# Performance work log

Hardware: AMD Instinct MI355X
Metric: run time of the kernel (lower is better)

Reference implementation:

```python
import jax, jax.numpy as jnp
import numpy as np

SIZE = 5
N_RADIAL = 4
EPS = 1e-5
PAD = [(3, 3)] * 3
# (scalar_in, scalar_out, vector) per Block, from features=[1,8,16,16,16,10]
DIMS = [(1, 8, 4), (8, 16, 12), (16, 16, 16), (16, 16, 16), (16, 10, 13)]


def _basis():
    # 5^3 grid of offsets, radial hat basis and angular (Cartesian) basis tensors
    o = jnp.arange(SIZE, dtype=jnp.float32) - (SIZE - 1) / 2.0
    X, Y, Z = jnp.meshgrid(o, o, o, indexing='ij')
    r = jnp.sqrt(X ** 2 + Y ** 2 + Z ** 2)
    hats = jnp.stack([jnp.clip(1.0 - jnp.abs(r - k), 0.0, None) for k in range(N_RADIAL)])  # [K,5,5,5]
    inv = jnp.where(r > 0, 1.0 / jnp.where(r > 0, r, 1.0), 0.0)
    xhat = jnp.stack([X * inv, Y * inv, Z * inv])  # [3,5,5,5], zero at origin
    mask = (r > 0).astype(jnp.float32)
    eye = jnp.eye(3, dtype=jnp.float32)
    e = np.zeros((3, 3, 3), np.float32)
    e[0, 1, 2] = e[1, 2, 0] = e[2, 0, 1] = 1.0
    e[0, 2, 1] = e[2, 1, 0] = e[1, 0, 2] = -1.0
    eps3 = jnp.asarray(e)
    a0 = eye[:, :, None, None, None] * jnp.ones_like(r)                      # J=0: delta_ij
    a1 = jnp.einsum('ijl,lxyz->ijxyz', eps3, xhat)                           # J=1: eps_ijl xhat_l
    a2 = xhat[:, None] * xhat[None, :] - eye[:, :, None, None, None] / 3.0 * mask  # J=2 traceless sym
    ang = jnp.stack([a0, a1, a2])  # [3,3,3,5,5,5]
    return hats, xhat, ang


def _conv(x, K, stride):
    return jax.lax.conv_general_dilated(x, K, (stride,) * 3, PAD,
                                        dimension_numbers=('NCDHW', 'OIDHW', 'NCDHW'))


def _bn3d(x, gamma, beta):
    m = x.mean((0, 2, 3, 4), keepdims=True)
    v = x.var((0, 2, 3, 4), keepdims=True)
    xn = (x - m) * jax.lax.rsqrt(v + EPS)
    return xn * gamma[None, :, None, None, None] + beta[None, :, None, None, None]


def _block(s, w1, wA, wB, bias, gamma, beta, relu, hats, xhat, ang):
    vec, s_in = w1.shape[0], w1.shape[1]
    s_out = wA.shape[0]
    # conv1: scalar -> vector, equivariant kernel K1[o*3+j, i] = xhat_j * sum_k w1[o,i,k] hat_k(r)
    R1 = jnp.einsum('oik,kxyz->oixyz', w1, hats)
    K1 = (xhat[None, :, None] * R1[:, None]).reshape(vec * 3, s_in, SIZE, SIZE, SIZE)
    v = _conv(s, K1, 2)  # [B, vec*3, D,H,W]
    B = v.shape[0]
    sp = v.shape[2:]
    # TensorProduct: per-channel outer product v_i v_j -> repr3x3 (9 comps)
    vr = v.reshape(B, vec, 3, *sp)
    t = (vr[:, :, :, None] * vr[:, :, None, :]).reshape(B, vec * 9, *sp)
    vt = jnp.concatenate([v, t], axis=1)
    # conv2: (repr3 ++ repr3x3) -> scalar
    RA = jnp.einsum('ovk,kxyz->ovxyz', wA, hats)
    KA = (RA[:, :, None] * xhat[None, None]).reshape(s_out, vec * 3, SIZE, SIZE, SIZE)
    RB = jnp.einsum('ovmk,kxyz->ovmxyz', wB, hats)
    KB = jnp.einsum('ovmxyz,mijxyz->ovijxyz', RB, ang).reshape(s_out, vec * 9, SIZE, SIZE, SIZE)
    K2 = jnp.concatenate([KA, KB], axis=1)
    out = _conv(vt, K2, 1)
    out = _bn3d(out, gamma, beta)  # scalar_batch_norm=True
    if relu:  # bias_relu flag
        out = jax.nn.relu(out + bias[None, :, None, None, None])
    return out


def _forward(x, params, gamma_out, beta_out):
    hats, xhat, ang = _basis()
    # bn_in, affine=False
    m = x.mean((0, 2, 3, 4), keepdims=True)
    v = x.var((0, 2, 3, 4), keepdims=True)
    s = (x - m) * jax.lax.rsqrt(v + EPS)
    n = len(params)
    for i, (w1, wA, wB, bias, gamma, beta) in enumerate(params):
        s = _block(s, w1, wA, wB, bias, gamma, beta, i < n - 1, hats, xhat, ang)
    pooled = s.mean((2, 3, 4))  # global average pool -> [B, classes]
    m = pooled.mean(0)
    v = pooled.var(0)
    return gamma_out * (pooled - m) * jax.lax.rsqrt(v + EPS) + beta_out


def setup_inputs() -> dict:
    key = jax.random.key(0)
    ks = iter(jax.random.split(key, 64))
    inp = {'x': jax.random.normal(next(ks), (32, 1, 64, 64, 64), dtype=jnp.float32)}
    for i, (si, so, ve) in enumerate(DIMS):
        inp[f'w1_{i}'] = jax.random.normal(next(ks), (ve, si, N_RADIAL), dtype=jnp.float32) * (si * 125) ** -0.5
        inp[f'wA_{i}'] = jax.random.normal(next(ks), (so, ve, N_RADIAL), dtype=jnp.float32) * (ve * 3 * 125) ** -0.5
        inp[f'wB_{i}'] = jax.random.normal(next(ks), (so, ve, 3, N_RADIAL), dtype=jnp.float32) * (ve * 9 * 125) ** -0.5
        inp[f'bias_{i}'] = jnp.zeros((so,), jnp.float32)
        inp[f'gamma_{i}'] = jnp.ones((so,), jnp.float32)
        inp[f'beta_{i}'] = jnp.zeros((so,), jnp.float32)
    inp['gamma_out'] = jnp.ones((10,), jnp.float32)
    inp['beta_out'] = jnp.zeros((10,), jnp.float32)
    return inp


def reference(x, w1_0, wA_0, wB_0, bias_0, gamma_0, beta_0,
              w1_1, wA_1, wB_1, bias_1, gamma_1, beta_1,
              w1_2, wA_2, wB_2, bias_2, gamma_2, beta_2,
              w1_3, wA_3, wB_3, bias_3, gamma_3, beta_3,
              w1_4, wA_4, wB_4, bias_4, gamma_4, beta_4,
              gamma_out, beta_out):
    params = [
        (w1_0, wA_0, wB_0, bias_0, gamma_0, beta_0),
        (w1_1, wA_1, wB_1, bias_1, gamma_1, beta_1),
        (w1_2, wA_2, wB_2, bias_2, gamma_2, beta_2),
        (w1_3, wA_3, wB_3, bias_3, gamma_3, beta_3),
        (w1_4, wA_4, wB_4, bias_4, gamma_4, beta_4),
    ]
    return _forward(x, params, gamma_out, beta_out)
```

## Files before the change

### kernel.cpp

```cpp
#include <hip/hip_runtime.h>
#include <math.h>

#define EPSF 1e-5f

typedef _Float16 f16;
typedef __attribute__((ext_vector_type(8))) _Float16 f16x8;
typedef __attribute__((ext_vector_type(4))) float f32x4;

__device__ __forceinline__ void tap_geom(int tap, float hats[4], float xh[3], float& mask) {
  int d = tap / 25, h = (tap / 5) % 5, w = tap % 5;
  float X = (float)(d - 2), Y = (float)(h - 2), Z = (float)(w - 2);
  float r = sqrtf(X * X + Y * Y + Z * Z);
#pragma unroll
  for (int k = 0; k < 4; ++k) hats[k] = fmaxf(1.0f - fabsf(r - (float)k), 0.0f);
  float inv = (r > 0.0f) ? (1.0f / r) : 0.0f;
  xh[0] = X * inv; xh[1] = Y * inv; xh[2] = Z * inv;
  mask = (r > 0.0f) ? 1.0f : 0.0f;
}

__global__ void build_k1(const float* __restrict__ w1, float* __restrict__ K1,
                         int VEC, int SIN) {
  int total = SIN * 125 * VEC;
  for (int idx = blockIdx.x * blockDim.x + threadIdx.x; idx < total;
       idx += gridDim.x * blockDim.x) {
    int cv = idx % VEC;
    int tap = (idx / VEC) % 125;
    int i = idx / (VEC * 125);
    float hats[4], xh[3], mask;
    tap_geom(tap, hats, xh, mask);
    float R = 0.f;
#pragma unroll
    for (int k = 0; k < 4; ++k) R += w1[(cv * SIN + i) * 4 + k] * hats[k];
    float* o = K1 + (long)idx * 4;
    o[0] = xh[0] * R; o[1] = xh[1] * R; o[2] = xh[2] * R; o[3] = 0.f;
  }
}

__global__ void build_k2c(const float* __restrict__ wA, const float* __restrict__ wB,
                          f16* __restrict__ K2, int VEC, int SOUT, int KS) {
  int total = 125 * KS * 64 * 8;
  for (int idx = blockIdx.x * blockDim.x + threadIdx.x; idx < total;
       idx += gridDim.x * blockDim.x) {
    int e = idx & 7;
    int lane = (idx >> 3) & 63;
    int ks = (idx >> 9) % KS;
    int tap = idx / (KS << 9);
    int n = lane & 15;
    int g = lane >> 4;
    int c = (ks * 4 + g) * 8 + e;
    float val = 0.f;
    if (n < SOUT && c < VEC * 12) {
      float hats[4], xh[3], mask;
      tap_geom(tap, hats, xh, mask);
      int cv = c / 12, comp = c % 12;
      if (comp < 3) {
        float RA = 0.f;
#pragma unroll
        for (int k = 0; k < 4; ++k) RA += wA[(n * VEC + cv) * 4 + k] * hats[k];
        val = RA * xh[comp];
      } else {
        int ij = comp - 3;
        int ii = ij / 3, jj = ij % 3;
        float RB[3];
#pragma unroll
        for (int m = 0; m < 3; ++m) {
          float r = 0.f;
#pragma unroll
          for (int k = 0; k < 4; ++k) r += wB[((n * VEC + cv) * 3 + m) * 4 + k] * hats[k];
          RB[m] = r;
        }
        float a0 = (ii == jj) ? 1.0f : 0.0f;
        float a1 = 0.0f;
        if (ii != jj) {
          int l = 3 - ii - jj;
          float sgn = (((jj - ii + 3) % 3) == 1) ? 1.0f : -1.0f;
          a1 = sgn * xh[l];
        }
        float a2 = xh[ii] * xh[jj] - ((ii == jj) ? (mask / 3.0f) : 0.0f);
        val = RB[0] * a0 + RB[1] * a1 + RB[2] * a2;
      }
    }
    K2[idx] = (f16)val;
  }
}

template <int SIN, int VEC, int CP8>
__global__ __launch_bounds__(256) void conv1_vt_x(const float* __restrict__ s,
                                                  const f32x4* __restrict__ K1,
                                                  f16* __restrict__ VT,
                                                  int Bc, int IS, int OS, int XG) {
  constexpr int NP = (VEC + 1) / 2;
  int iss = IS * IS * IS;
  long total = (long)Bc * OS * OS * XG * NP;
  for (long idx = blockIdx.x * (long)blockDim.x + threadIdx.x; idx < total;
       idx += gridDim.x * (long)blockDim.x) {
    int xg = (int)(idx % XG);
    int pp = (int)((idx / XG) % NP);
    int y  = (int)((idx / ((long)XG * NP)) % OS);
    int z  = (int)((idx / ((long)XG * NP * OS)) % OS);
    int b  = (int)(idx / ((long)XG * NP * OS * OS));
    int x0 = xg * 4;
    int cv0 = 2 * pp;
    int cv1 = (2 * pp + 1 < VEC) ? (2 * pp + 1) : (VEC - 1);

    float acc[2][3][4];
#pragma unroll
    for (int p = 0; p < 2; ++p)
#pragma unroll
      for (int c = 0; c < 3; ++c)
#pragma unroll
        for (int t = 0; t < 4; ++t) acc[p][c][t] = 0.f;

    const float* sb = s + (long)b * SIN * iss;
    const f32x4* kb = K1;
    for (int i = 0; i < SIN; ++i) {
      for (int d = 0; d < 5; ++d) {
        int iz = 2 * z - 3 + d;
        if ((unsigned)iz >= (unsigned)IS) continue;
        for (int h = 0; h < 5; ++h) {
          int iy = 2 * y - 3 + h;
          if ((unsigned)iy >= (unsigned)IS) continue;
          const float* srow = sb + (iz * IS + iy) * IS;
          float sv[11];
#pragma unroll
          for (int m = 0; m < 11; ++m) {
            int xi = 2 * x0 - 3 + m;
            bool ok = (unsigned)xi < (unsigned)IS;
            sv[m] = ok ? srow[ok ? xi : 0] : 0.f;
          }
          const f32x4* krow = kb + (d * 25 + h * 5) * VEC;
#pragma unroll
          for (int w = 0; w < 5; ++w) {
            f32x4 k0 = krow[w * VEC + cv0];
            f32x4 k1 = krow[w * VEC + cv1];
#pragma unroll
            for (int t = 0; t < 4; ++t) {
              float sx = sv[2 * t + w];
              acc[0][0][t] = fmaf(sx, k0[0], acc[0][0][t]);
              acc[0][1][t] = fmaf(sx, k0[1], acc[0][1][t]);
              acc[0][2][t] = fmaf(sx, k0[2], acc[0][2][t]);
              acc[1][0][t] = fmaf(sx, k1[0], acc[1][0][t]);
              acc[1][1][t] = fmaf(sx, k1[1], acc[1][1][t]);
              acc[1][2][t] = fmaf(sx, k1[2], acc[1][2][t]);
            }
          }
        }
      }
      sb += iss;
      kb += 125 * VEC;
    }

    long ybase = (((long)(b * OS + z) * OS + y) * CP8) * (long)OS * 8;
    int cg0 = pp * 3;
#pragma unroll
    for (int t = 0; t < 4; ++t) {
      int x = x0 + t;
      if (x >= OS) continue;
      float a00 = acc[0][0][t], a01 = acc[0][1][t], a02 = acc[0][2][t];
      float a10 = acc[1][0][t], a11 = acc[1][1][t], a12 = acc[1][2][t];
      float v0[12] = {a00, a01, a02,
                      a00 * a00, a00 * a01, a00 * a02,
                      a01 * a00, a01 * a01, a01 * a02,
                      a02 * a00, a02 * a01, a02 * a02};
      float v1[12] = {a10, a11, a12,
                      a10 * a10, a10 * a11, a10 * a12,
                      a11 * a10, a11 * a11, a11 * a12,
                      a12 * a10, a12 * a11, a12 * a12};
      f16x8 pk0, pk1, pk2;
#pragma unroll
      for (int e = 0; e < 8; ++e) pk0[e] = (f16)v0[e];
#pragma unroll
      for (int e = 0; e < 4; ++e) { pk1[e] = (f16)v0[8 + e]; pk1[4 + e] = (f16)v1[e]; }
#pragma unroll
      for (int e = 0; e < 8; ++e) pk2[e] = (f16)v1[4 + e];
      long rowbase = ybase + (long)x * 8;
      *(f16x8*)(VT + rowbase + (long)(cg0 + 0) * OS * 8) = pk0;
      *(f16x8*)(VT + rowbase + (long)(cg0 + 1) * OS * 8) = pk1;
      *(f16x8*)(VT + rowbase + (long)(cg0 + 2) * OS * 8) = pk2;
    }
  }
}

template <int SIN, int NSL, int VEC>
__global__ __launch_bounds__(256) void conv1_part(const float* __restrict__ s,
                                                  const f32x4* __restrict__ K1,
                                                  float* __restrict__ Vp,
                                                  int Bc, int IS, int OS, int XG, int XP) {
  constexpr int NP = (VEC + 1) / 2;
  constexpr int SLC = SIN / NSL;
  constexpr int V3 = VEC * 3;
  int iss = IS * IS * IS;
  long total = (long)Bc * OS * OS * NP * NSL * XG;
  for (long idx = blockIdx.x * (long)blockDim.x + threadIdx.x; idx < total;
       idx += gridDim.x * (long)blockDim.x) {
    int xg = (int)(idx % XG);
    int sl = (int)((idx / XG) % NSL);
    int pp = (int)((idx / ((long)XG * NSL)) % NP);
    int y  = (int)((idx / ((long)XG * NSL * NP)) % OS);
    int z  = (int)((idx / ((long)XG * NSL * NP * OS)) % OS);
    int b  = (int)(idx / ((long)XG * NSL * NP * OS * OS));
    int x0 = xg * 4;
    int cv0 = 2 * pp;
    int cv1 = (2 * pp + 1 < VEC) ? (2 * pp + 1) : (VEC - 1);

    float acc[2][3][4];
#pragma unroll
    for (int p = 0; p < 2; ++p)
#pragma unroll
      for (int c = 0; c < 3; ++c)
#pragma unroll
        for (int t = 0; t < 4; ++t) acc[p][c][t] = 0.f;

    const float* sb = s + ((long)b * SIN + sl * SLC) * iss;
    const f32x4* kb = K1 + (long)(sl * SLC) * 125 * VEC;
    for (int i = 0; i < SLC; ++i) {
      for (int d = 0; d < 5; ++d) {
        int iz = 2 * z - 3 + d;
        if ((unsigned)iz >= (unsigned)IS) continue;
        for (int h = 0; h < 5; ++h) {
          int iy = 2 * y - 3 + h;
          if ((unsigned)iy >= (unsigned)IS) continue;
          const float* srow = sb + (iz * IS + iy) * IS;
          float sv[11];
#pragma unroll
          for (int m = 0; m < 11; ++m) {
            int xi = 2 * x0 - 3 + m;
            bool ok = (unsigned)xi < (unsigned)IS;
            sv[m] = ok ? srow[ok ? xi : 0] : 0.f;
          }
          const f32x4* krow = kb + (d * 25 + h * 5) * VEC;
#pragma unroll
          for (int w = 0; w < 5; ++w) {
            f32x4 k0 = krow[w * VEC + cv0];
            f32x4 k1 = krow[w * VEC + cv1];
#pragma unroll
            for (int t = 0; t < 4; ++t) {
              float sx = sv[2 * t + w];
              acc[0][0][t] = fmaf(sx, k0[0], acc[0][0][t]);
              acc[0][1][t] = fmaf(sx, k0[1], acc[0][1][t]);
              acc[0][2][t] = fmaf(sx, k0[2], acc[0][2][t]);
              acc[1][0][t] = fmaf(sx, k1[0], acc[1][0][t]);
              acc[1][1][t] = fmaf(sx, k1[1], acc[1][1][t]);
              acc[1][2][t] = fmaf(sx, k1[2], acc[1][2][t]);
            }
          }
        }
      }
      sb += iss;
      kb += 125 * VEC;
    }

    long row = (((long)sl * Bc + b) * OS + z) * OS + y;
    float* base = Vp + row * V3 * XP + x0;
#pragma unroll
    for (int p = 0; p < 2; ++p) {
      int cv = p ? cv1 : cv0;
#pragma unroll
      for (int c = 0; c < 3; ++c) {
        f32x4 st = {acc[p][c][0], acc[p][c][1], acc[p][c][2], acc[p][c][3]};
        *(f32x4*)(base + (long)(cv * 3 + c) * XP) = st;
      }
    }
  }
}

template <int VEC, int NSL, int CP8>
__global__ __launch_bounds__(256) void vt_pack(const float* __restrict__ Vp,
                                               f16* __restrict__ VT,
                                               int Bc, int OS, int XP) {
  constexpr int NP = (VEC + 1) / 2;
  constexpr int V3 = VEC * 3;
  long total = (long)Bc * OS * OS * NP * OS;
  for (long idx = blockIdx.x * (long)blockDim.x + threadIdx.x; idx < total;
       idx += gridDim.x * (long)blockDim.x) {
    int x  = (int)(idx % OS);
    int pp = (int)((idx / OS) % NP);
    int y  = (int)((idx / ((long)OS * NP)) % OS);
    int z  = (int)((idx / ((long)OS * NP * OS)) % OS);
    int b  = (int)(idx / ((long)OS * NP * OS * OS));
    int cv0 = 2 * pp;
    int cv1 = (2 * pp + 1 < VEC) ? (2 * pp + 1) : (VEC - 1);

    float a[6] = {0.f, 0.f, 0.f, 0.f, 0.f, 0.f};
    for (int sl = 0; sl < NSL; ++sl) {
      long row = (((long)sl * Bc + b) * OS + z) * OS + y;
      const float* base = Vp + row * V3 * XP + x;
#pragma unroll
      for (int c = 0; c < 3; ++c) {
        a[c]     += base[(long)(cv0 * 3 + c) * XP];
        a[3 + c] += base[(long)(cv1 * 3 + c) * XP];
      }
    }
    float a00 = a[0], a01 = a[1], a02 = a[2];
    float a10 = a[3], a11 = a[4], a12 = a[5];
    float v0[12] = {a00, a01, a02,
                    a00 * a00, a00 * a01, a00 * a02,
                    a01 * a00, a01 * a01, a01 * a02,
                    a02 * a00, a02 * a01, a02 * a02};
    float v1[12] = {a10, a11, a12,
                    a10 * a10, a10 * a11, a10 * a12,
                    a11 * a10, a11 * a11, a11 * a12,
                    a12 * a10, a12 * a11, a12 * a12};
    f16x8 pk0, pk1, pk2;
#pragma unroll
    for (int e = 0; e < 8; ++e) pk0[e] = (f16)v0[e];
#pragma unroll
    for (int e = 0; e < 4; ++e) { pk1[e] = (f16)v0[8 + e]; pk1[4 + e] = (f16)v1[e]; }
#pragma unroll
    for (int e = 0; e < 8; ++e) pk2[e] = (f16)v1[4 + e];
    long rowbase = (((long)(b * OS + z) * OS + y) * CP8) * (long)OS * 8 + (long)x * 8;
    int cg0 = pp * 3;
    *(f16x8*)(VT + rowbase + (long)(cg0 + 0) * OS * 8) = pk0;
    *(f16x8*)(VT + rowbase + (long)(cg0 + 1) * OS * 8) = pk1;
    *(f16x8*)(VT + rowbase + (long)(cg0 + 2) * OS * 8) = pk2;
  }
}

template <int CP8, int SOUT, int ZT>
__global__ __launch_bounds__(256) void conv2_mfma(const f16* __restrict__ VT,
                                                  const f16* __restrict__ K2,
                                                  float* __restrict__ out,
                                                  int Bc, int IS, int OS, int XG, int ZG) {
  constexpr int KS = CP8 / 4;
  constexpr int NU = ZT + 4;
  int nwg = gridDim.x;
  int orig = blockIdx.x;
  int q = nwg >> 3, r = nwg & 7;
  int xcd = orig & 7, sub = orig >> 3;
  int swz = (xcd < r ? xcd * (q + 1) : r * (q + 1) + (xcd - r) * q) + sub;
  int wid = swz * (blockDim.x >> 6) + ((int)threadIdx.x >> 6);
  int lane = threadIdx.x & 63;
  int total = Bc * ZG * OS * XG;
  if (wid >= total) return;
  int xg = wid % XG;
  int y  = (wid / XG) % OS;
  int zg = (wid / (XG * OS)) % ZG;
  int b  = wid / (XG * OS * ZG);
  int z0 = zg * ZT;
  int x0 = xg * 16;
  int lm = lane & 15;
  int g  = lane >> 4;

  f32x4 acc[ZT];
#pragma unroll
  for (int t = 0; t < ZT; ++t) acc[t] = (f32x4){0.f, 0.f, 0.f, 0.f};

  const f16* kl = K2 + ((long)lane << 3);

  for (int h = 0; h < 5; ++h) {
    int yi = y - 3 + h;
    if ((unsigned)yi >= (unsigned)IS) continue;
    const f16* base[NU];
    bool zok[NU];
#pragma unroll
    for (int u = 0; u < NU; ++u) {
      int zi = z0 - 3 + u;
      zok[u] = (unsigned)zi < (unsigned)IS;
      int zc = zok[u] ? zi : 0;
      base[u] = VT + (((long)(b * IS + zc) * IS + yi) * CP8) * (long)IS * 8;
    }
    int hw = h * 5;
#pragma unroll 1
    for (int w = 0; w < 5; ++w) {
      int xi = x0 + lm - 3 + w;
      bool xok = (unsigned)xi < (unsigned)IS;
#pragma unroll
      for (int ks = 0; ks < KS; ++ks) {
        f16x8 bf[5];
#pragma unroll
        for (int d = 0; d < 5; ++d)
          bf[d] = *(const f16x8*)(kl + ((long)((d * 25 + hw + w) * KS + ks) << 9));
        f16x8 af[NU];
#pragma unroll
        for (int u = 0; u < NU; ++u) {
          af[u] = (f16x8){};
          if (zok[u] && xok)
            af[u] = *(const f16x8*)(base[u] + ((ks * 4 + g) * IS + xi) * 8);
        }
#pragma unroll
        for (int u = 0; u < NU; ++u) {
#pragma unroll
          for (int t = 0; t < ZT; ++t) {
            int d = u - t;
            if (d >= 0 && d <= 4)
              acc[t] = __builtin_amdgcn_mfma_f32_16x16x32_f16(af[u], bf[d], acc[t], 0, 0, 0);
          }
        }
      }
    }
  }
  if (lm < SOUT) {
    int oss = OS * OS * OS;
#pragma unroll
    for (int t = 0; t < ZT; ++t) {
      int z = z0 + t;
      if (z < OS) {
        float* op = out + ((long)b * SOUT + lm) * oss + (z * OS + y) * OS;
#pragma unroll
        for (int r2 = 0; r2 < 4; ++r2) {
          int xm = x0 + g * 4 + r2;
          if (xm < OS) op[xm] = acc[t][r2];
        }
      }
    }
  }
}

__global__ void stats1(const float* __restrict__ a, float* __restrict__ part,
                       int B, int C, int ss, int nblk) {
  int c = blockIdx.y;
  int tid = threadIdx.x;
  float s = 0.f, s2 = 0.f;
  for (int b = 0; b < B; ++b) {
    const float* ab = a + ((long)b * C + c) * ss;
    for (int p = blockIdx.x * blockDim.x + tid; p < ss; p += nblk * blockDim.x) {
      float x = ab[p];
      s += x;
      s2 += x * x;
    }
  }
  __shared__ float sh[256], sh2[256];
  sh[tid] = s; sh2[tid] = s2;
  __syncthreads();
  for (int off = 128; off > 0; off >>= 1) {
    if (tid < off) { sh[tid] += sh[tid + off]; sh2[tid] += sh2[tid + off]; }
    __syncthreads();
  }
  if (tid == 0) {
    part[(c * nblk + blockIdx.x) * 2 + 0] = sh[0];
    part[(c * nblk + blockIdx.x) * 2 + 1] = sh2[0];
  }
}

__global__ void stats2(const float* __restrict__ part, float* __restrict__ stats,
                       int nblk, float invn) {
  int c = blockIdx.x;
  int tid = threadIdx.x;
  float s = 0.f, s2 = 0.f;
  for (int i = tid; i < nblk; i += blockDim.x) {
    s += part[(c * nblk + i) * 2 + 0];
    s2 += part[(c * nblk + i) * 2 + 1];
  }
  __shared__ float sh[256], sh2[256];
  sh[tid] = s; sh2[tid] = s2;
  __syncthreads();
  for (int off = 128; off > 0; off >>= 1) {
    if (tid < off) { sh[tid] += sh[tid + off]; sh2[tid] += sh2[tid + off]; }
    __syncthreads();
  }
  if (tid == 0) {
    float m = sh[0] * invn;
    float var = sh2[0] * invn - m * m;
    stats[c * 2 + 0] = m;
    stats[c * 2 + 1] = 1.0f / sqrtf(var + EPSF);
  }
}

__global__ void bn_apply(const float* __restrict__ in, float* __restrict__ out,
                         const float* __restrict__ stats, const float* __restrict__ g,
                         const float* __restrict__ be, const float* __restrict__ bias,
                         int C, int ss, int relu) {
  int bc = blockIdx.y;
  int c = bc % C;
  float m = stats[c * 2 + 0];
  float r = stats[c * 2 + 1];
  float ga = g ? g[c] : 1.f;
  float bb = be ? be[c] : 0.f;
  float bi = bias ? bias[c] : 0.f;
  const float* ip = in + (long)bc * ss;
  float* op = out + (long)bc * ss;
  for (int p = blockIdx.x * blockDim.x + threadIdx.x; p < ss; p += gridDim.x * blockDim.x) {
    float xn = (ip[p] - m) * r * ga + bb;
    if (relu) xn = fmaxf(xn + bi, 0.f);
    op[p] = xn;
  }
}

__global__ void pool_k(const float* __restrict__ in, float* __restrict__ pooled, int ss) {
  int bc = blockIdx.x;
  int tid = threadIdx.x;
  const float* p = in + (long)bc * ss;
  float s = 0.f;
  for (int e = tid; e < ss; e += blockDim.x) s += p[e];
  __shared__ float sh[256];
  sh[tid] = s;
  __syncthreads();
  for (int off = 128; off > 0; off >>= 1) {
    if (tid < off) sh[tid] += sh[tid + off];
    __syncthreads();
  }
  if (tid == 0) pooled[bc] = sh[0] / (float)ss;
}

__global__ void final_bn(const float* __restrict__ pooled, const float* __restrict__ g,
                         const float* __restrict__ be, float* __restrict__ out,
                         int B, int C) {
  int tid = threadIdx.x;
  __shared__ float mv[16][2];
  if (tid < C) {
    float s = 0.f, s2 = 0.f;
    for (int b = 0; b < B; ++b) {
      float x = pooled[b * C + tid];
      s += x;
      s2 += x * x;
    }
    float m = s / (float)B;
    float var = s2 / (float)B - m * m;
    mv[tid][0] = m;
    mv[tid][1] = 1.0f / sqrtf(var + EPSF);
  }
  __syncthreads();
  for (int i = tid; i < B * C; i += blockDim.x) {
    int c = i % C;
    out[i] = g[c] * (pooled[i] - mv[c][0]) * mv[c][1] + be[c];
  }
}

extern "C" void kernel_launch(void* const* d_in, const int* in_sizes, int n_in,
                              void* d_out, int out_size, void* d_ws, size_t ws_size,
                              hipStream_t stream) {
  (void)in_sizes; (void)n_in; (void)out_size; (void)ws_size;
  const float* x = (const float*)d_in[0];
  const float* w1[5]; const float* wA[5]; const float* wB[5];
  const float* bias[5]; const float* gam[5]; const float* bet[5];
  for (int i = 0; i < 5; ++i) {
    w1[i]  = (const float*)d_in[1 + i * 6 + 0];
    wA[i]  = (const float*)d_in[1 + i * 6 + 1];
    wB[i]  = (const float*)d_in[1 + i * 6 + 2];
    bias[i]= (const float*)d_in[1 + i * 6 + 3];
    gam[i] = (const float*)d_in[1 + i * 6 + 4];
    bet[i] = (const float*)d_in[1 + i * 6 + 5];
  }
  const float* gamma_out = (const float*)d_in[31];
  const float* beta_out  = (const float*)d_in[32];
  float* out = (float*)d_out;

  float* A     = (float*)d_ws;
  float* Bb    = A + 8388608;
  float* V     = Bb + 10976000;
  float* K1    = V + 13799808;
  float* K2    = K1 + 128000;
  float* part  = K2 + 384000;
  float* stats = part + 16 * 256 * 2;
  float* pooled= stats + 64;
  f16* VT  = (f16*)V;
  f16* K2h = (f16*)K2;

  const int NB = 256;
  const int Bn = 32;
  const int ZT = 4;

  {
    int ss = 64 * 64 * 64;
    stats1<<<dim3(NB, 1), 256, 0, stream>>>(x, part, Bn, 1, ss, NB);
    stats2<<<1, 256, 0, stream>>>(part, stats, NB, 1.0f / (float)(Bn * (long)ss));
    int gx = (ss + 255) / 256;
    bn_apply<<<dim3(gx, Bn), 256, 0, stream>>>(x, A, stats, nullptr, nullptr, nullptr, 1, ss, 0);
  }

  const int SINs[5]  = {1, 8, 16, 16, 16};
  const int SOUTs[5] = {8, 16, 16, 16, 10};
  const int VECs[5]  = {4, 12, 16, 16, 13};
  const int ISs[5]   = {64, 35, 21, 14, 10};
  const int VSs[5]   = {33, 19, 12, 8, 6};
  const int OSs[5]   = {35, 21, 14, 10, 8};
  const int CP8s[5]  = {8, 24, 24, 24, 24};
  const int CHKs[5]  = {8, 16, 32, 32, 32};
  const int NPs[5]   = {2, 6, 8, 8, 7};

  float* sbuf = A;
  for (int i = 0; i < 5; ++i) {
    float* obuf = (i % 2 == 0) ? Bb : A;
    int IS = ISs[i], VS = VSs[i], OS = OSs[i];
    int VEC = VECs[i], SIN = SINs[i], SOUT = SOUTs[i];

    { int t = SIN * 125 * VEC;
      build_k1<<<(t + 255) / 256, 256, 0, stream>>>(w1[i], K1, VEC, SIN); }

    int CP8 = CP8s[i];
    int KS = CP8 / 4;
    int CHK = CHKs[i];
    int XG = (OS + 15) / 16;
    int ZG = (OS + ZT - 1) / ZT;
    int XG1 = (VS + 3) / 4;
    int XP1 = XG1 * 4;
    { int t = 125 * KS * 512;
      build_k2c<<<(t + 255) / 256, 256, 0, stream>>>(wA[i], wB[i], K2h, VEC, SOUT, KS); }
    for (int b0 = 0; b0 < Bn; b0 += CHK) {
      int bc = CHK;
      const float* sp = sbuf + (long)b0 * SIN * IS * IS * IS;
      float* op = obuf + (long)b0 * SOUT * OS * OS * OS;
      long waves = (long)bc * ZG * OS * XG;
      int g2 = (int)((waves * 64 + 255) / 256);
      if (i <= 1) {
        long t1 = (long)bc * VS * VS * XG1 * NPs[i];
        int g1 = (int)((t1 + 255) / 256);
        if (i == 0) {
          conv1_vt_x<1, 4, 8><<<g1, 256, 0, stream>>>(sp, (const f32x4*)K1, VT, bc, IS, VS, XG1);
          conv2_mfma<8, 8, ZT><<<g2, 256, 0, stream>>>(VT, K2h, op, bc, VS, OS, XG, ZG);
        } else {
          conv1_vt_x<8, 12, 24><<<g1, 256, 0, stream>>>(sp, (const f32x4*)K1, VT, bc, IS, VS, XG1);
          conv2_mfma<24, 16, ZT><<<g2, 256, 0, stream>>>(VT, K2h, op, bc, VS, OS, XG, ZG);
        }
      } else {
        float* Vp = obuf;
        long tA = (long)bc * VS * VS * NPs[i] * 4 * XG1;
        int gA = (int)((tA + 255) / 256);
        long tB = (long)bc * VS * VS * NPs[i] * VS;
        int gB = (int)((tB + 255) / 256);
        switch (i) {
          case 2:
            conv1_part<16, 4, 16><<<gA, 256, 0, stream>>>(sp, (const f32x4*)K1, Vp, bc, IS, VS, XG1, XP1);
            vt_pack<16, 4, 24><<<gB, 256, 0, stream>>>(Vp, VT, bc, VS, XP1);
            conv2_mfma<24, 16, ZT><<<g2, 256, 0, stream>>>(VT, K2h, op, bc, VS, OS, XG, ZG);
            break;
          case 3:
            conv1_part<16, 4, 16><<<gA, 256, 0, stream>>>(sp, (const f32x4*)K1, Vp, bc, IS, VS, XG1, XP1);
            vt_pack<16, 4, 24><<<gB, 256, 0, stream>>>(Vp, VT, bc, VS, XP1);
            conv2_mfma<24, 16, ZT><<<g2, 256, 0, stream>>>(VT, K2h, op, bc, VS, OS, XG, ZG);
            break;
          case 4:
            conv1_part<16, 4, 13><<<gA, 256, 0, stream>>>(sp, (const f32x4*)K1, Vp, bc, IS, VS, XG1, XP1);
            vt_pack<13, 4, 24><<<gB, 256, 0, stream>>>(Vp, VT, bc, VS, XP1);
            conv2_mfma<24, 10, ZT><<<g2, 256, 0, stream>>>(VT, K2h, op, bc, VS, OS, XG, ZG);
            break;
        }
      }
    }

    { int ss = OS * OS * OS;
      stats1<<<dim3(NB, SOUT), 256, 0, stream>>>(obuf, part, Bn, SOUT, ss, NB);
      stats2<<<SOUT, 256, 0, stream>>>(part, stats, NB, 1.0f / (float)((long)Bn * ss));
      int gx = (ss + 255) / 256;
      bn_apply<<<dim3(gx, Bn * SOUT), 256, 0, stream>>>(obuf, obuf, stats, gam[i], bet[i],
                                                        bias[i], SOUT, ss, (i < 4) ? 1 : 0);
    }
    sbuf = obuf;
  }

  pool_k<<<Bn * 10, 256, 0, stream>>>(sbuf, pooled, 8 * 8 * 8);
  final_bn<<<1, 64, 0, stream>>>(pooled, gamma_out, beta_out, out, Bn, 10);
}
```

Baseline: 3.521 ms.

## Restructure conv1 for late blocks as per-position all-channel kernel, unchunk batch

For blocks 2-4, conv1 now assigns one output position and one input-channel slice to each thread and accumulates all vec*3 output channels, reading a new channel-contiguous K1 layout. It writes Vp in a position-major layout that vt_pack2 reduces across slices. The batch is processed in one launch set instead of per-chunk loops, and blocks 3-4 use more input-channel slices. The aim is to cut launch count and uniform-broadcast the kernel weights across threads. The cost is large per-thread register accumulators (up to 48) and no x-reuse of input loads.

```diff
diff --git a/kernel.cpp b/kernel.cpp
--- a/kernel.cpp
+++ b/kernel.cpp
@@ -33,6 +33,25 @@
     for (int k = 0; k < 4; ++k) R += w1[(cv * SIN + i) * 4 + k] * hats[k];
     float* o = K1 + (long)idx * 4;
     o[0] = xh[0] * R; o[1] = xh[1] * R; o[2] = xh[2] * R; o[3] = 0.f;
+  }
+}
+
+__global__ void build_k1b(const float* __restrict__ w1, float* __restrict__ K1,
+                          int VEC, int SIN) {
+  int OC3 = VEC * 3;
+  int total = SIN * 125 * OC3;
+  for (int idx = blockIdx.x * blockDim.x + threadIdx.x; idx < total;
+       idx += gridDim.x * blockDim.x) {
+    int o = idx % OC3;
+    int tap = (idx / OC3) % 125;
+    int i = idx / (OC3 * 125);
+    int cv = o / 3, j = o % 3;
+    float hats[4], xh[3], mask;
+    tap_geom(tap, hats, xh, mask);
+    float R = 0.f;
+#pragma unroll
+    for (int k = 0; k < 4; ++k) R += w1[(cv * SIN + i) * 4 + k] * hats[k];
+    K1[idx] = xh[j] * R;
   }
 }
 
@@ -182,113 +201,96 @@
 }
 
 template <int SIN, int NSL, int VEC>
-__global__ __launch_bounds__(256) void conv1_part(const float* __restrict__ s,
-                                                  const f32x4* __restrict__ K1,
-                                                  float* __restrict__ Vp,
-                                                  int Bc, int IS, int OS, int XG, int XP) {
-  constexpr int NP = (VEC + 1) / 2;
+__global__ __launch_bounds__(256) void conv1_pos(const float* __restrict__ s,
+                                                 const float* __restrict__ K1,
+                                                 float* __restrict__ Vp,
+                                                 int Bc, int IS, int OS) {
+  constexpr int OC3 = VEC * 3;
   constexpr int SLC = SIN / NSL;
-  constexpr int V3 = VEC * 3;
   int iss = IS * IS * IS;
-  long total = (long)Bc * OS * OS * NP * NSL * XG;
+  int oss = OS * OS * OS;
+  long POS = (long)Bc * oss;
+  long total = POS * NSL;
   for (long idx = blockIdx.x * (long)blockDim.x + threadIdx.x; idx < total;
        idx += gridDim.x * (long)blockDim.x) {
-    int xg = (int)(idx % XG);
-    int sl = (int)((idx / XG) % NSL);
-    int pp = (int)((idx / ((long)XG * NSL)) % NP);
-    int y  = (int)((idx / ((long)XG * NSL * NP)) % OS);
-    int z  = (int)((idx / ((long)XG * NSL * NP * OS)) % OS);
-    int b  = (int)(idx / ((long)XG * NSL * NP * OS * OS));
-    int x0 = xg * 4;
+    long pos = idx % POS;
+    int sl = (int)(idx / POS);
+    int x = (int)(pos % OS);
+    int y = (int)((pos / OS) % OS);
+    int z = (int)((pos / (OS * OS)) % OS);
+    int b = (int)(pos / oss);
+
+    int zc[5], yc[5], xc[5];
+    bool zv[5], yv[5], xv[5];
+#pragma unroll
+    for (int d = 0; d < 5; ++d) {
+      int iz = 2 * z - 3 + d; zv[d] = (unsigned)iz < (unsigned)IS; zc[d] = zv[d] ? iz : 0;
+      int iy = 2 * y - 3 + d; yv[d] = (unsigned)iy < (unsigned)IS; yc[d] = yv[d] ? iy : 0;
+      int ix = 2 * x - 3 + d; xv[d] = (unsigned)ix < (unsigned)IS; xc[d] = xv[d] ? ix : 0;
+    }
+
+    float acc[OC3];
+#pragma unroll
+    for (int o = 0; o < OC3; ++o) acc[o] = 0.f;
+
+    const float* sb = s + ((long)b * SIN + sl * SLC) * iss;
+    const float* kb = K1 + (long)(sl * SLC) * 125 * OC3;
+    for (int i = 0; i < SLC; ++i) {
+      for (int d = 0; d < 5; ++d) {
+        for (int h = 0; h < 5; ++h) {
+          const float* srow = sb + (zc[d] * IS + yc[h]) * IS;
+          bool vzh = zv[d] && yv[h];
+          float sv[5];
+#pragma unroll
+          for (int w = 0; w < 5; ++w)
+            sv[w] = (vzh && xv[w]) ? srow[xc[w]] : 0.f;
+          const float* kr = kb + (d * 25 + h * 5) * OC3;
+#pragma unroll
+          for (int w = 0; w < 5; ++w) {
+            float sx = sv[w];
+#pragma unroll
+            for (int o = 0; o < OC3; ++o)
+              acc[o] = fmaf(sx, kr[w * OC3 + o], acc[o]);
+          }
+        }
+      }
+      sb += iss;
+      kb += 125 * OC3;
+    }
+
+    float* vp = Vp + (long)sl * OC3 * POS + pos;
+#pragma unroll
+    for (int o = 0; o < OC3; ++o) vp[(long)o * POS] = acc[o];
+  }
+}
+
+template <int VEC, int NSL, int CP8>
+__global__ __launch_bounds__(256) void vt_pack2(const float* __restrict__ Vp,
+                                                f16* __restrict__ VT,
+                                                int Bc, int OS) {
+  constexpr int NP = (VEC + 1) / 2;
+  constexpr int OC3 = VEC * 3;
+  int oss = OS * OS * OS;
+  long POS = (long)Bc * oss;
+  long total = POS * NP;
+  for (long idx = blockIdx.x * (long)blockDim.x + threadIdx.x; idx < total;
+       idx += gridDim.x * (long)blockDim.x) {
+    long pos = idx % POS;
+    int pp = (int)(idx / POS);
+    int x = (int)(pos % OS);
+    int y = (int)((pos / OS) % OS);
+    int z = (int)((pos / (OS * OS)) % OS);
+    int b = (int)(pos / oss);
     int cv0 = 2 * pp;
     int cv1 = (2 * pp + 1 < VEC) ? (2 * pp + 1) : (VEC - 1);
 
-    float acc[2][3][4];
-#pragma unroll
-    for (int p = 0; p < 2; ++p)
-#pragma unroll
-      for (int c = 0; c < 3; ++c)
-#pragma unroll
-        for (int t = 0; t < 4; ++t) acc[p][c][t] = 0.f;
-
-    const float* sb = s + ((long)b * SIN + sl * SLC) * iss;
-    const f32x4* kb = K1 + (long)(sl * SLC) * 125 * VEC;
-    for (int i = 0; i < SLC; ++i) {
-      for (int d = 0; d < 5; ++d) {
-        int iz = 2 * z - 3 + d;
-        if ((unsigned)iz >= (unsigned)IS) continue;
-        for (int h = 0; h < 5; ++h) {
-          int iy = 2 * y - 3 + h;
-          if ((unsigned)iy >= (unsigned)IS) continue;
-          const float* srow = sb + (iz * IS + iy) * IS;
-          float sv[11];
-#pragma unroll
-          for (int m = 0; m < 11; ++m) {
-            int xi = 2 * x0 - 3 + m;
-            bool ok = (unsigned)xi < (unsigned)IS;
-            sv[m] = ok ? srow[ok ? xi : 0] : 0.f;
-          }
-          const f32x4* krow = kb + (d * 25 + h * 5) * VEC;
-#pragma unroll
-          for (int w = 0; w < 5; ++w) {
-            f32x4 k0 = krow[w * VEC + cv0];
-            f32x4 k1 = krow[w * VEC + cv1];
-#pragma unroll
-            for (int t = 0; t < 4; ++t) {
-              float sx = sv[2 * t + w];
-              acc[0][0][t] = fmaf(sx, k0[0], acc[0][0][t]);
-              acc[0][1][t] = fmaf(sx, k0[1], acc[0][1][t]);
-              acc[0][2][t] = fmaf(sx, k0[2], acc[0][2][t]);
-              acc[1][0][t] = fmaf(sx, k1[0], acc[1][0][t]);
-              acc[1][1][t] = fmaf(sx, k1[1], acc[1][1][t]);
-              acc[1][2][t] = fmaf(sx, k1[2], acc[1][2][t]);
-            }
-          }
-        }
-      }
-      sb += iss;
-      kb += 125 * VEC;
-    }
-
-    long row = (((long)sl * Bc + b) * OS + z) * OS + y;
-    float* base = Vp + row * V3 * XP + x0;
-#pragma unroll
-    for (int p = 0; p < 2; ++p) {
-      int cv = p ? cv1 : cv0;
-#pragma unroll
-      for (int c = 0; c < 3; ++c) {
-        f32x4 st = {acc[p][c][0], acc[p][c][1], acc[p][c][2], acc[p][c][3]};
-        *(f32x4*)(base + (long)(cv * 3 + c) * XP) = st;
-      }
-    }
-  }
-}
-
-template <int VEC, int NSL, int CP8>
-__global__ __launch_bounds__(256) void vt_pack(const float* __restrict__ Vp,
-                                               f16* __restrict__ VT,
-                                               int Bc, int OS, int XP) {
-  constexpr int NP = (VEC + 1) / 2;
-  constexpr int V3 = VEC * 3;
-  long total = (long)Bc * OS * OS * NP * OS;
-  for (long idx = blockIdx.x * (long)blockDim.x + threadIdx.x; idx < total;
-       idx += gridDim.x * (long)blockDim.x) {
-    int x  = (int)(idx % OS);
-    int pp = (int)((idx / OS) % NP);
-    int y  = (int)((idx / ((long)OS * NP)) % OS);
-    int z  = (int)((idx / ((long)OS * NP * OS)) % OS);
-    int b  = (int)(idx / ((long)OS * NP * OS * OS));
-    int cv0 = 2 * pp;
-    int cv1 = (2 * pp + 1 < VEC) ? (2 * pp + 1) : (VEC - 1);
-
     float a[6] = {0.f, 0.f, 0.f, 0.f, 0.f, 0.f};
     for (int sl = 0; sl < NSL; ++sl) {
-      long row = (((long)sl * Bc + b) * OS + z) * OS + y;
-      const float* base = Vp + row * V3 * XP + x;
+      const float* base = Vp + (long)sl * OC3 * POS + pos;
 #pragma unroll
       for (int c = 0; c < 3; ++c) {
-        a[c]     += base[(long)(cv0 * 3 + c) * XP];
-        a[3 + c] += base[(long)(cv1 * 3 + c) * XP];
+        a[c]     += base[(long)(cv0 * 3 + c) * POS];
+        a[3 + c] += base[(long)(cv1 * 3 + c) * POS];
       }
     }
     float a00 = a[0], a01 = a[1], a02 = a[2];
@@ -574,25 +576,24 @@
     int IS = ISs[i], VS = VSs[i], OS = OSs[i];
     int VEC = VECs[i], SIN = SINs[i], SOUT = SOUTs[i];
 
-    { int t = SIN * 125 * VEC;
-      build_k1<<<(t + 255) / 256, 256, 0, stream>>>(w1[i], K1, VEC, SIN); }
-
     int CP8 = CP8s[i];
     int KS = CP8 / 4;
     int CHK = CHKs[i];
     int XG = (OS + 15) / 16;
     int ZG = (OS + ZT - 1) / ZT;
     int XG1 = (VS + 3) / 4;
-    int XP1 = XG1 * 4;
     { int t = 125 * KS * 512;
       build_k2c<<<(t + 255) / 256, 256, 0, stream>>>(wA[i], wB[i], K2h, VEC, SOUT, KS); }
-    for (int b0 = 0; b0 < Bn; b0 += CHK) {
-      int bc = CHK;
-      const float* sp = sbuf + (long)b0 * SIN * IS * IS * IS;
-      float* op = obuf + (long)b0 * SOUT * OS * OS * OS;
-      long waves = (long)bc * ZG * OS * XG;
-      int g2 = (int)((waves * 64 + 255) / 256);
-      if (i <= 1) {
+
+    if (i <= 1) {
+      { int t = SIN * 125 * VEC;
+        build_k1<<<(t + 255) / 256, 256, 0, stream>>>(w1[i], K1, VEC, SIN); }
+      for (int b0 = 0; b0 < Bn; b0 += CHK) {
+        int bc = CHK;
+        const float* sp = sbuf + (long)b0 * SIN * IS * IS * IS;
+        float* op = obuf + (long)b0 * SOUT * OS * OS * OS;
+        long waves = (long)bc * ZG * OS * XG;
+        int g2 = (int)((waves * 64 + 255) / 256);
         long t1 = (long)bc * VS * VS * XG1 * NPs[i];
         int g1 = (int)((t1 + 255) / 256);
         if (i == 0) {
@@ -602,28 +603,41 @@
           conv1_vt_x<8, 12, 24><<<g1, 256, 0, stream>>>(sp, (const f32x4*)K1, VT, bc, IS, VS, XG1);
           conv2_mfma<24, 16, ZT><<<g2, 256, 0, stream>>>(VT, K2h, op, bc, VS, OS, XG, ZG);
         }
-      } else {
-        float* Vp = obuf;
-        long tA = (long)bc * VS * VS * NPs[i] * 4 * XG1;
-        int gA = (int)((tA + 255) / 256);
-        long tB = (long)bc * VS * VS * NPs[i] * VS;
-        int gB = (int)((tB + 255) / 256);
-        switch (i) {
-          case 2:
-            conv1_part<16, 4, 16><<<gA, 256, 0, stream>>>(sp, (const f32x4*)K1, Vp, bc, IS, VS, XG1, XP1);
-            vt_pack<16, 4, 24><<<gB, 256, 0, stream>>>(Vp, VT, bc, VS, XP1);
-            conv2_mfma<24, 16, ZT><<<g2, 256, 0, stream>>>(VT, K2h, op, bc, VS, OS, XG, ZG);
-            break;
-          case 3:
-            conv1_part<16, 4, 16><<<gA, 256, 0, stream>>>(sp, (const f32x4*)K1, Vp, bc, IS, VS, XG1, XP1);
-            vt_pack<16, 4, 24><<<gB, 256, 0, stream>>>(Vp, VT, bc, VS, XP1);
-            conv2_mfma<24, 16, ZT><<<g2, 256, 0, stream>>>(VT, K2h, op, bc, VS, OS, XG, ZG);
-            break;
-          case 4:
-            conv1_part<16, 4, 13><<<gA, 256, 0, stream>>>(sp, (const f32x4*)K1, Vp, bc, IS, VS, XG1, XP1);
-            vt_pack<13, 4, 24><<<gB, 256, 0, stream>>>(Vp, VT, bc, VS, XP1);
-            conv2_mfma<24, 10, ZT><<<g2, 256, 0, stream>>>(VT, K2h, op, bc, VS, OS, XG, ZG);
-            break;
+      }
+    } else {
+      { int t = SIN * 125 * VEC * 3;
+        build_k1b<<<(t + 255) / 256, 256, 0, stream>>>(w1[i], K1, VEC, SIN); }
+      int bc = Bn;
+      const float* sp = sbuf;
+      float* op = obuf;
+      float* Vp = obuf;
+      long POS = (long)bc * VS * VS * VS;
+      long waves = (long)bc * ZG * OS * XG;
+      int g2 = (int)((waves * 64 + 255) / 256);
+      switch (i) {
+        case 2: {
+          long tA = POS * 4; int gA = (int)((tA + 255) / 256);
+          long tB = POS * 8; int gB = (int)((tB + 255) / 256);
+          conv1_pos<16, 4, 16><<<gA, 256, 0, stream>>>(sp, K1, Vp, bc, IS, VS);
+          vt_pack2<16, 4, 24><<<gB, 256, 0, stream>>>(Vp, VT, bc, VS);
+          conv2_mfma<24, 16, ZT><<<g2, 256, 0, stream>>>(VT, K2h, op, bc, VS, OS, XG, ZG);
+          break;
+        }
+        case 3: {
+          long tA = POS * 8; int gA = (int)((tA + 255) / 256);
+          long tB = POS * 8; int gB = (int)((tB + 255) / 256);
+          conv1_pos<16, 8, 16><<<gA, 256, 0, stream>>>(sp, K1, Vp, bc, IS, VS);
+          vt_pack2<16, 8, 24><<<gB, 256, 0, stream>>>(Vp, VT, bc, VS);
+          conv2_mfma<24, 16, ZT><<<g2, 256, 0, stream>>>(VT, K2h, op, bc, VS, OS, XG, ZG);
+          break;
+        }
+        case 4: {
+          long tA = POS * 8; int gA = (int)((tA + 255) / 256);
+          long tB = POS * 7; int gB = (int)((tB + 255) / 256);
+          conv1_pos<16, 8, 13><<<gA, 256, 0, stream>>>(sp, K1, Vp, bc, IS, VS);
+          vt_pack2<13, 8, 24><<<gB, 256, 0, stream>>>(Vp, VT, bc, VS);
+          conv2_mfma<24, 10, ZT><<<g2, 256, 0, stream>>>(VT, K2h, op, bc, VS, OS, XG, ZG);
+          break;
         }
       }
     }
```

Measured after the change: 4.107 ms. 1.17x slower.
